# Kernel tuning notes

Hardware: AMD Instinct MI355X
Metric: run time of the kernel (lower is better)

The kernel has to match this reference:

```python
import jax, jax.numpy as jnp
import numpy as np

L = 5; F = 16; K = 32; R_CUT = 5.0; N_TYPES = 10
A = 10000  # n_atoms
P = 50000  # n_atom_pairs


def cg_coeff(l1, l2, l3):
    # Deterministic stand-in for Clebsch-Gordan coefficients (cgc arg of the layer).
    rs = np.random.RandomState(1000 + l1 * 100 + l2 * 10 + l3)
    return jnp.asarray(rs.standard_normal((2 * l1 + 1, 2 * l2 + 1, 2 * l3 + 1)).astype(np.float32))


def setup_inputs() -> dict:
    key = jax.random.key(0)
    ks = jax.random.split(key, 16)
    inp = {}
    for l in range(L):
        inp[f"c{l}"] = jax.random.normal(ks[l], (A, F, 2 * l + 1), jnp.float32)
    inp["R"] = jax.random.uniform(ks[5], (A, 3), jnp.float32) * 3.0  # positions in a box -> most d < r_cut
    inp["w_rad"] = jax.random.normal(ks[6], (L, K, F), jnp.float32) * 0.1
    inp["weight"] = jax.random.normal(ks[7], (N_TYPES * N_TYPES, L, F, F), jnp.float32) * (1.0 / np.sqrt(F))
    inp["s_collapse"] = jax.random.normal(ks[8], (3, F), jnp.float32) * 0.1
    inp["p_collapse"] = jax.random.normal(ks[9], (2, F), jnp.float32) * 0.1
    inp["d_collapse"] = jax.random.normal(ks[10], (1, F), jnp.float32) * 0.1
    inp["Z"] = jax.random.randint(ks[11], (A,), 0, N_TYPES)
    inp["atom_pair_indices"] = jax.random.randint(ks[12], (P, 2), 0, A)
    inp["atom_idx"] = jnp.arange(P)
    return inp


def reference(c0, c1, c2, c3, c4, R, w_rad, weight, s_collapse, p_collapse, d_collapse,
              Z, atom_pair_indices, atom_idx):
    c = [c0, c1, c2, c3, c4]
    i, j = atom_pair_indices[:, 0], atom_pair_indices[:, 1]
    # pairwise displacement / distance
    Rij = R[i] - R[j]                                    # (P,3)
    d = jnp.linalg.norm(Rij, axis=-1)                    # (P,)
    # Pairmix: smooth radial basis with cosine cutoff, per-l projection K->F
    n = jnp.arange(1, K + 1, dtype=jnp.float32)
    env = 0.5 * (jnp.cos(jnp.pi * jnp.clip(d, 0.0, R_CUT) / R_CUT) + 1.0) * (d < R_CUT)
    rbf = jnp.sin(n[None, :] * jnp.pi * d[:, None] / R_CUT) * env[:, None]   # (P,K)
    g = jnp.einsum('pk,lkf->lpf', rbf, w_rad)            # (L,P,F)
    c_out = [g[l][:, :, None] * (c[l][i] + c[l][j]) for l in range(L)]        # (P,F,2l+1)
    # atom-type-pair weights (symmetrized)
    sel = atom_pair_indices[atom_idx]                    # (P,2)
    t1, t2 = Z[sel[:, 0]], Z[sel[:, 1]]
    gw = weight[t1 * N_TYPES + t2] + weight[t2 * N_TYPES + t1]               # (P,L,F,F)
    c_out = [jnp.einsum('pbc,pcm->pbm', gw[:, l], c_out[l]) for l in range(L)]
    # CG tensor-product expansion into (l1,l2) blocks
    collapses = [s_collapse, p_collapse, d_collapse]
    Mblk = {}
    for l1 in range(3):
        for l2 in range(l1 + 1):
            Mx = jnp.zeros((P, 2 * l1 + 1, 2 * l2 + 1, F), jnp.float32)
            for l3 in range(l1 - l2, l1 + l2 + 1):
                Mx = Mx + jnp.einsum('mna,pfa->pmnf', cg_coeff(l1, l2, l3), c_out[l3])
            Mx = jnp.einsum('pmnf,af,bf->pmnab', Mx, collapses[l1], collapses[l2])
            a, b = collapses[l1].shape[0], collapses[l2].shape[0]
            Mblk[(l1, l2)] = Mx.reshape(P, (2 * l1 + 1) * a, (2 * l2 + 1) * b)
    T = lambda x: jnp.transpose(x, (0, 2, 1))
    r1 = jnp.concatenate([Mblk[(0, 0)], Mblk[(1, 0)], Mblk[(2, 0)]], axis=1)   # (P,14,3)
    r2 = jnp.concatenate([T(Mblk[(1, 0)]), Mblk[(1, 1)], Mblk[(2, 1)]], axis=1)  # (P,14,6)
    r3 = jnp.concatenate([T(Mblk[(2, 0)]), T(Mblk[(2, 1)]), Mblk[(2, 2)]], axis=1)  # (P,14,5)
    return jnp.concatenate([r1, r2, r3], axis=2)         # (P,14,14)
```

## Files before the change

### kernel.cpp

```cpp
#include <hip/hip_runtime.h>
#include <cstdint>

#define PI_F 3.14159265358979323846f

namespace cgc {

constexpr double csqrt(double x) {
  if (x <= 0.0) return 0.0;
  double m = x; int e = 0;
  while (m >= 4.0) { m *= 0.25; e++; }
  while (m < 1.0) { m *= 4.0; e--; }
  double g = 1.5;
  for (int i = 0; i < 16; i++) g = 0.5 * (g + m / g);
  double s = g;
  if (e > 0) for (int i = 0; i < e; i++) s *= 2.0;
  else       for (int i = 0; i < -e; i++) s *= 0.5;
  return s;
}

constexpr double clog(double x) {
  int k = 0;
  double m = x;
  while (m < 0.7071067811865476) { m *= 2.0; k--; }
  while (m > 1.4142135623730951) { m *= 0.5; k++; }
  double t = (m - 1.0) / (m + 1.0), t2 = t * t, s = 0.0, p = t;
  for (int i = 0; i < 27; i++) { s += p / (double)(2 * i + 1); p *= t2; }
  return 2.0 * s + (double)k * 0.6931471805599453;
}

struct RS { uint32_t mt[624]; int mti; bool has; double g; };

constexpr void rs_seed(RS& r, uint32_t s) {
  for (int i = 0; i < 624; i++) { r.mt[i] = s; s = 1812433253u * (s ^ (s >> 30)) + (uint32_t)i + 1u; }
  r.mti = 624; r.has = false; r.g = 0.0;
}
constexpr uint32_t rs_next(RS& r) {
  if (r.mti >= 624) {
    for (int i = 0; i < 624; i++) {
      uint32_t y = (r.mt[i] & 0x80000000u) | (r.mt[(i + 1) % 624] & 0x7fffffffu);
      r.mt[i] = r.mt[(i + 397) % 624] ^ (y >> 1) ^ ((y & 1u) ? 0x9908b0dfu : 0u);
    }
    r.mti = 0;
  }
  uint32_t y = r.mt[r.mti++];
  y ^= y >> 11; y ^= (y << 7) & 0x9d2c5680u; y ^= (y << 15) & 0xefc60000u; y ^= y >> 18;
  return y;
}
constexpr double rs_dbl(RS& r) {
  uint32_t a = rs_next(r) >> 5, b = rs_next(r) >> 6;
  return ((double)a * 67108864.0 + (double)b) / 9007199254740992.0;
}
constexpr double rs_gauss(RS& r) {
  if (r.has) { r.has = false; return r.g; }
  double x1 = 0, x2 = 0, r2 = 0;
  do {
    x1 = 2.0 * rs_dbl(r) - 1.0;
    x2 = 2.0 * rs_dbl(r) - 1.0;
    r2 = x1 * x1 + x2 * x2;
  } while (r2 >= 1.0 || r2 == 0.0);
  double f = csqrt(-2.0 * clog(r2) / r2);
  r.g = f * x1; r.has = true;
  return f * x2;
}

struct Tab { float v[228]; };

constexpr Tab gen(int l1, int l2, int l3) {
  Tab t{};
  RS r{};
  rs_seed(r, (uint32_t)(1000 + l1 * 100 + l2 * 10 + l3));
  int sz = (2 * l1 + 1) * (2 * l2 + 1) * (2 * l3 + 1);
  for (int k = 0; k < sz; k++) t.v[k] = (float)rs_gauss(r);
  return t;
}

constexpr Tab T000 = gen(0,0,0);
constexpr Tab T101 = gen(1,0,1);
constexpr Tab T110 = gen(1,1,0);
constexpr Tab T111 = gen(1,1,1);
constexpr Tab T112 = gen(1,1,2);
constexpr Tab T202 = gen(2,0,2);
constexpr Tab T211 = gen(2,1,1);
constexpr Tab T212 = gen(2,1,2);
constexpr Tab T213 = gen(2,1,3);
constexpr Tab T220 = gen(2,2,0);
constexpr Tab T221 = gen(2,2,1);
constexpr Tab T222 = gen(2,2,2);
constexpr Tab T223 = gen(2,2,3);
constexpr Tab T224 = gen(2,2,4);

struct alignas(16) Stage {
  int tabD[133 * 4];
  float cg[966];
  uint32_t tabC[133];
};

constexpr Stage make_stage() {
  Stage S{};
  const Tab* tabs[14] = {&T000,&T101,&T110,&T111,&T112,&T202,&T211,&T212,&T213,
                         &T220,&T221,&T222,&T223,&T224};
  const int KL[14][3] = {{0,0,0},{1,0,1},{1,1,0},{1,1,1},{1,1,2},{2,0,2},{2,1,1},
                         {2,1,2},{2,1,3},{2,2,0},{2,2,1},{2,2,2},{2,2,3},{2,2,4}};
  const int kBk[6][2] = {{0,0},{1,0},{1,1},{2,0},{2,1},{2,2}};

  int cgbase[6] = {}, dbase[6] = {}, xlenA[6] = {};
  int off = 0, doff = 0;
  for (int bk = 0; bk < 6; bk++) {
    int l1 = kBk[bk][0], l2 = kBk[bk][1];
    int M = 2 * l1 + 1, N = 2 * l2 + 1;
    int Ar = (l1 == 0) ? 3 : (l1 == 1) ? 2 : 1;
    int Br = (l2 == 0) ? 3 : (l2 == 1) ? 2 : 1;
    int xs[25] = {}, xl3[25] = {}, xa[25] = {};
    int cnt = 0;
    for (int l3 = l1 - l2; l3 <= l1 + l2; l3++)
      for (int a = 0; a < 2 * l3 + 1; a++) {
        xs[cnt] = l3 * l3 + a; xl3[cnt] = l3; xa[cnt] = a; cnt++;
      }
    int xlen = cnt;
    xlenA[bk] = xlen; cgbase[bk] = off; dbase[bk] = doff;
    for (int mn = 0; mn < M * N; mn++)
      for (int xi = 0; xi < xlen; xi++) {
        int l3 = xl3[xi], K3 = 2 * l3 + 1, ti = 0;
        for (int c = 0; c < 14; c++)
          if (KL[c][0] == l1 && KL[c][1] == l2 && KL[c][2] == l3) ti = c;
        S.cg[off + mn * xlen + xi] = tabs[ti]->v[mn * K3 + xa[xi]];
      }
    off += M * N * xlen;
    for (int q = 0; q < Ar * Br; q++) {
      int a = q / Br, b = q % Br;
      int u = (l1 == 0) ? a : (l1 == 1) ? 3 + a : 5;
      int v = (l2 == 0) ? b : (l2 == 1) ? 3 + b : 5;
      for (int xi = 0; xi < xlen; xi++)
        S.tabC[doff + q * xlen + xi] = (uint32_t)(u | (v << 4) | (xs[xi] << 8));
    }
    doff += Ar * Br * xlen;
  }
  const int ord[6] = {5, 4, 2, 3, 1, 0};
  int ei = 0;
  for (int bo = 0; bo < 6; bo++) {
    int bk = ord[bo];
    int l1 = kBk[bk][0], l2 = kBk[bk][1];
    int M = 2 * l1 + 1, N = 2 * l2 + 1;
    int Ar = (l1 == 0) ? 3 : (l1 == 1) ? 2 : 1;
    int Br = (l2 == 0) ? 3 : (l2 == 1) ? 2 : 1;
    int rb1 = (l1 == 0) ? 0 : (l1 == 1) ? 3 : 9;
    int rb2 = (l2 == 0) ? 0 : (l2 == 1) ? 3 : 9;
    int colDim = N * Br, xlen = xlenA[bk];
    for (int e = 0; e < M * N * Ar * Br; e++) {
      int b = e % Br, t2 = e / Br;
      int a = t2 % Ar; t2 /= Ar;
      int n = t2 % N, m = t2 / N;
      int mn = m * N + n, q = a * Br + b;
      int ri = e / colDim, ci = e % colDim;
      int p1 = (rb1 + ri) * 14 + (rb2 + ci);
      int p2 = (l1 == l2) ? p1 : ((rb2 + ci) * 14 + (rb1 + ri));
      S.tabD[4 * ei + 0] = (cgbase[bk] + mn * xlen) | (xlen << 16);
      S.tabD[4 * ei + 1] = dbase[bk] + q * xlen;
      S.tabD[4 * ei + 2] = p1;
      S.tabD[4 * ei + 3] = p2;
      ei++;
    }
  }
  return S;
}

constexpr Stage ST = make_stage();

}

__device__ const cgc::Stage g_tab = cgc::ST;

#define PSTRIDE 536

__global__ __launch_bounds__(256, 4) void outlayer_kernel(
    const float* __restrict__ c0, const float* __restrict__ c1,
    const float* __restrict__ c2, const float* __restrict__ c3,
    const float* __restrict__ c4, const float* __restrict__ R,
    const float* __restrict__ w_rad, const float* __restrict__ weight,
    const float* __restrict__ s_colg, const float* __restrict__ p_colg,
    const float* __restrict__ d_colg, const int* __restrict__ Z,
    const int* __restrict__ api, const int* __restrict__ aidx,
    float* __restrict__ out) {
  __shared__ float s_wrad[2560];
  __shared__ __align__(16) float s_cg[966];
  __shared__ __align__(16) float s_w6[36 * 16];
  __shared__ __align__(16) float s_buf[16 * PSTRIDE];
  __shared__ int s_tabC[133];
  __shared__ __align__(16) int4 s_tabD[133];

  const int tid = threadIdx.x;

#pragma unroll
  for (int t = 0; t < 10; t++) s_wrad[tid + t * 256] = w_rad[tid + t * 256];
  for (int e = tid; e < 966; e += 256) s_cg[e] = g_tab.cg[e];
  for (int e = tid; e < 133; e += 256) {
    s_tabC[e] = (int)g_tab.tabC[e];
    s_tabD[e] = ((const int4*)g_tab.tabD)[e];
  }
  for (int idx = tid; idx < 576; idx += 256) {
    int comb = idx >> 4, f = idx & 15;
    int u = comb / 6, v = comb % 6;
    float cu = (u < 3) ? s_colg[u * 16 + f] : (u < 5) ? p_colg[(u - 3) * 16 + f] : d_colg[f];
    float cv = (v < 3) ? s_colg[v * 16 + f] : (v < 5) ? p_colg[(v - 3) * 16 + f] : d_colg[f];
    s_w6[comb * 16 + ((f + 4 * (comb >> 1)) & 15)] = cu * cv;
  }
  __syncthreads();

  const int grp = tid >> 4;
  const int lane = tid & 15;
  const int p = blockIdx.x * 16 + grp;
  float* sb = s_buf + grp * PSTRIDE;
  float* sbD = sb + 400;

  const int i = api[2 * p], j = api[2 * p + 1];
  const int ai = aidx[p];
  const int t1 = Z[api[2 * ai]], t2 = Z[api[2 * ai + 1]];

  float dx = R[3 * i + 0] - R[3 * j + 0];
  float dy = R[3 * i + 1] - R[3 * j + 1];
  float dz = R[3 * i + 2] - R[3 * j + 2];
  float d = sqrtf(dx * dx + dy * dy + dz * dz);
  float env = 0.0f;
  if (d < 5.0f) env = 0.5f * (__cosf(PI_F * d * 0.2f) + 1.0f);
  float th = PI_F * d * 0.2f;
  float rlo = __sinf((float)(lane + 1) * th) * env;
  float rhi = __sinf((float)(lane + 17) * th) * env;

  float gl[5] = {0.f, 0.f, 0.f, 0.f, 0.f};
#pragma unroll
  for (int k = 0; k < 16; k++) {
    float rv = __shfl(rlo, k, 16);
#pragma unroll
    for (int l = 0; l < 5; l++) gl[l] += rv * s_wrad[l * 512 + k * 16 + lane];
  }
#pragma unroll
  for (int k = 0; k < 16; k++) {
    float rv = __shfl(rhi, k, 16);
#pragma unroll
    for (int l = 0; l < 5; l++) gl[l] += rv * s_wrad[l * 512 + (k + 16) * 16 + lane];
  }

  const float* cl[5] = {c0, c1, c2, c3, c4};
#pragma unroll
  for (int l = 0; l < 5; l++) {
    const int nm = 2 * l + 1;
    const float* ci = cl[l] + ((size_t)i * 16 + lane) * nm;
    const float* cj = cl[l] + ((size_t)j * 16 + lane) * nm;
    float* hb = sb + 16 * l * l;
#pragma unroll
    for (int m = 0; m < 2 * l + 1; m++)
      hb[m * 16 + lane] = gl[l] * (ci[m] + cj[m]);
  }
  __builtin_amdgcn_wave_barrier();

  float co[25];
#pragma unroll
  for (int x = 0; x < 25; x++) co[x] = 0.f;
  const float* w1 = weight + (size_t)(t1 * 10 + t2) * 1280 + lane * 16;
  const float* w2 = weight + (size_t)(t2 * 10 + t1) * 1280 + lane * 16;
#pragma unroll
  for (int l = 0; l < 5; l++) {
    float gwreg[16];
#pragma unroll
    for (int cq = 0; cq < 4; cq++) {
      float4 a4 = *(const float4*)(w1 + l * 256 + cq * 4);
      float4 b4 = *(const float4*)(w2 + l * 256 + cq * 4);
      gwreg[cq * 4 + 0] = a4.x + b4.x;
      gwreg[cq * 4 + 1] = a4.y + b4.y;
      gwreg[cq * 4 + 2] = a4.z + b4.z;
      gwreg[cq * 4 + 3] = a4.w + b4.w;
    }
#pragma unroll
    for (int m = 0; m < 2 * l + 1; m++) {
      const float* hb = &sb[16 * l * l + m * 16];
      float acc = co[l * l + m];
#pragma unroll
      for (int cq = 0; cq < 4; cq++) {
        float4 h4 = *(const float4*)(hb + cq * 4);
        acc += gwreg[cq * 4 + 0] * h4.x + gwreg[cq * 4 + 1] * h4.y +
               gwreg[cq * 4 + 2] * h4.z + gwreg[cq * 4 + 3] * h4.w;
      }
      co[l * l + m] = acc;
    }
  }
  __builtin_amdgcn_wave_barrier();

#pragma unroll
  for (int x = 0; x < 25; x++) sb[x * 16 + ((lane + 4 * (x >> 1)) & 15)] = co[x];
  __builtin_amdgcn_wave_barrier();

#pragma unroll
  for (int it = 0; it < 9; it++) {
    int t = it * 16 + lane;
    if (t < 133) {
      int pc = s_tabC[t];
      int u = pc & 15, v = (pc >> 4) & 15, x = pc >> 8;
      int comb = u * 6 + v;
      int rotW = 4 * (comb >> 1), rotC = 4 * (x >> 1);
      const float* wrow = &s_w6[comb * 16];
      const float* crow = &sb[x * 16];
      float acc = 0.f;
#pragma unroll
      for (int q = 0; q < 4; q++) {
        float4 wv = *(const float4*)&wrow[(4 * q + rotW) & 15];
        float4 cv = *(const float4*)&crow[(4 * q + rotC) & 15];
        acc += wv.x * cv.x + wv.y * cv.y + wv.z * cv.z + wv.w * cv.w;
      }
      sbD[t] = acc;
    }
  }
  __builtin_amdgcn_wave_barrier();

#pragma unroll
  for (int it = 0; it < 9; it++) {
    int t = it * 16 + lane;
    if (t < 133) {
      int4 td = s_tabD[t];
      int goff = td.x & 0xffff, len = td.x >> 16, doff = td.y;
      float acc = 0.f;
      for (int xi = 0; xi < len; xi++) acc += s_cg[goff + xi] * sbD[doff + xi];
      sb[td.z] = acc;
      sb[td.w] = acc;
    }
  }
  __builtin_amdgcn_wave_barrier();

  float* outp = out + (size_t)p * 196;
#pragma unroll
  for (int r = 0; r < 4; r++) {
    int idx = r * 16 + lane;
    if (idx < 49) {
      float4 v = *(const float4*)&sb[idx * 4];
      *(float4*)(outp + idx * 4) = v;
    }
  }
}

extern "C" void kernel_launch(void* const* d_in, const int* in_sizes, int n_in,
                              void* d_out, int out_size, void* d_ws, size_t ws_size,
                              hipStream_t stream) {
  (void)in_sizes; (void)n_in; (void)out_size; (void)d_ws; (void)ws_size;

  const float* c0 = (const float*)d_in[0];
  const float* c1 = (const float*)d_in[1];
  const float* c2 = (const float*)d_in[2];
  const float* c3 = (const float*)d_in[3];
  const float* c4 = (const float*)d_in[4];
  const float* R = (const float*)d_in[5];
  const float* w_rad = (const float*)d_in[6];
  const float* weight = (const float*)d_in[7];
  const float* s_col = (const float*)d_in[8];
  const float* p_col = (const float*)d_in[9];
  const float* d_col = (const float*)d_in[10];
  const int* Z = (const int*)d_in[11];
  const int* api = (const int*)d_in[12];
  const int* aidx = (const int*)d_in[13];

  dim3 grid(3125), block(256);
  hipLaunchKernelGGL(outlayer_kernel, grid, block, 0, stream,
                     c0, c1, c2, c3, c4, R, w_rad, weight, s_col, p_col, d_col,
                     Z, api, aidx, (float*)d_out);
}
```

Before: 182.2 us.

## Drop shared-memory staging of tables and radial weights; pad CG rows to float4

Stops copying w_rad, the CG coefficients and the index tables into shared memory at block start. Those values are now read straight from global/constant memory, and each lane computes all 32 radial sines itself instead of shuffling them across lanes. The CG and intermediate D rows are padded to multiples of four so the final contraction can use float4 loads, and the padding in the per-pair buffer is zeroed first. This shrinks LDS use and the block prologue, at the cost of more global loads through the cache and 32 sine evaluations per lane instead of 2.

```diff
diff --git a/kernel.cpp b/kernel.cpp
--- a/kernel.cpp
+++ b/kernel.cpp
@@ -90,8 +90,8 @@
 constexpr Tab T224 = gen(2,2,4);
 
 struct alignas(16) Stage {
+  float cgP[1104];
   int tabD[133 * 4];
-  float cg[966];
   uint32_t tabC[133];
 };
 
@@ -103,7 +103,7 @@
                          {2,1,2},{2,1,3},{2,2,0},{2,2,1},{2,2,2},{2,2,3},{2,2,4}};
   const int kBk[6][2] = {{0,0},{1,0},{1,1},{2,0},{2,1},{2,2}};
 
-  int cgbase[6] = {}, dbase[6] = {}, xlenA[6] = {};
+  int cgbase[6] = {}, dbase[6] = {}, xlenA[6] = {}, cgs[6] = {}, dss[6] = {};
   int off = 0, doff = 0;
   for (int bk = 0; bk < 6; bk++) {
     int l1 = kBk[bk][0], l2 = kBk[bk][1];
@@ -117,23 +117,40 @@
         xs[cnt] = l3 * l3 + a; xl3[cnt] = l3; xa[cnt] = a; cnt++;
       }
     int xlen = cnt;
-    xlenA[bk] = xlen; cgbase[bk] = off; dbase[bk] = doff;
+    int pstride = ((xlen + 3) / 4) * 4;
+    xlenA[bk] = xlen; cgs[bk] = pstride; dss[bk] = pstride;
+    cgbase[bk] = off; dbase[bk] = doff;
     for (int mn = 0; mn < M * N; mn++)
       for (int xi = 0; xi < xlen; xi++) {
         int l3 = xl3[xi], K3 = 2 * l3 + 1, ti = 0;
         for (int c = 0; c < 14; c++)
           if (KL[c][0] == l1 && KL[c][1] == l2 && KL[c][2] == l3) ti = c;
-        S.cg[off + mn * xlen + xi] = tabs[ti]->v[mn * K3 + xa[xi]];
-      }
-    off += M * N * xlen;
-    for (int q = 0; q < Ar * Br; q++) {
-      int a = q / Br, b = q % Br;
-      int u = (l1 == 0) ? a : (l1 == 1) ? 3 + a : 5;
-      int v = (l2 == 0) ? b : (l2 == 1) ? 3 + b : 5;
-      for (int xi = 0; xi < xlen; xi++)
-        S.tabC[doff + q * xlen + xi] = (uint32_t)(u | (v << 4) | (xs[xi] << 8));
-    }
-    doff += Ar * Br * xlen;
+        S.cgP[off + mn * pstride + xi] = tabs[ti]->v[mn * K3 + xa[xi]];
+      }
+    off += M * N * pstride;
+    doff += Ar * Br * pstride;
+  }
+  {
+    int t = 0;
+    for (int bk = 0; bk < 6; bk++) {
+      int l1 = kBk[bk][0], l2 = kBk[bk][1];
+      int Ar = (l1 == 0) ? 3 : (l1 == 1) ? 2 : 1;
+      int Br = (l2 == 0) ? 3 : (l2 == 1) ? 2 : 1;
+      for (int q = 0; q < Ar * Br; q++) {
+        int a = q / Br, b = q % Br;
+        int u = (l1 == 0) ? a : (l1 == 1) ? 3 + a : 5;
+        int v = (l2 == 0) ? b : (l2 == 1) ? 3 + b : 5;
+        int comb = u * 6 + v;
+        int xi = 0;
+        for (int l3 = l1 - l2; l3 <= l1 + l2; l3++)
+          for (int a3 = 0; a3 < 2 * l3 + 1; a3++) {
+            int x = l3 * l3 + a3;
+            int pos = dbase[bk] + q * dss[bk] + xi;
+            S.tabC[t++] = (uint32_t)(comb | (x << 8) | (pos << 16));
+            xi++;
+          }
+      }
+    }
   }
   const int ord[6] = {5, 4, 2, 3, 1, 0};
   int ei = 0;
@@ -145,7 +162,7 @@
     int Br = (l2 == 0) ? 3 : (l2 == 1) ? 2 : 1;
     int rb1 = (l1 == 0) ? 0 : (l1 == 1) ? 3 : 9;
     int rb2 = (l2 == 0) ? 0 : (l2 == 1) ? 3 : 9;
-    int colDim = N * Br, xlen = xlenA[bk];
+    int colDim = N * Br;
     for (int e = 0; e < M * N * Ar * Br; e++) {
       int b = e % Br, t2 = e / Br;
       int a = t2 % Ar; t2 /= Ar;
@@ -154,8 +171,8 @@
       int ri = e / colDim, ci = e % colDim;
       int p1 = (rb1 + ri) * 14 + (rb2 + ci);
       int p2 = (l1 == l2) ? p1 : ((rb2 + ci) * 14 + (rb1 + ri));
-      S.tabD[4 * ei + 0] = (cgbase[bk] + mn * xlen) | (xlen << 16);
-      S.tabD[4 * ei + 1] = dbase[bk] + q * xlen;
+      S.tabD[4 * ei + 0] = ((cgbase[bk] + mn * cgs[bk]) / 4) | ((cgs[bk] / 4) << 16);
+      S.tabD[4 * ei + 1] = dbase[bk] + q * dss[bk];
       S.tabD[4 * ei + 2] = p1;
       S.tabD[4 * ei + 3] = p2;
       ei++;
@@ -170,7 +187,7 @@
 
 __device__ const cgc::Stage g_tab = cgc::ST;
 
-#define PSTRIDE 536
+#define PSTRIDE 600
 
 __global__ __launch_bounds__(256, 4) void outlayer_kernel(
     const float* __restrict__ c0, const float* __restrict__ c1,
@@ -181,22 +198,11 @@
     const float* __restrict__ d_colg, const int* __restrict__ Z,
     const int* __restrict__ api, const int* __restrict__ aidx,
     float* __restrict__ out) {
-  __shared__ float s_wrad[2560];
-  __shared__ __align__(16) float s_cg[966];
   __shared__ __align__(16) float s_w6[36 * 16];
   __shared__ __align__(16) float s_buf[16 * PSTRIDE];
-  __shared__ int s_tabC[133];
-  __shared__ __align__(16) int4 s_tabD[133];
 
   const int tid = threadIdx.x;
 
-#pragma unroll
-  for (int t = 0; t < 10; t++) s_wrad[tid + t * 256] = w_rad[tid + t * 256];
-  for (int e = tid; e < 966; e += 256) s_cg[e] = g_tab.cg[e];
-  for (int e = tid; e < 133; e += 256) {
-    s_tabC[e] = (int)g_tab.tabC[e];
-    s_tabD[e] = ((const int4*)g_tab.tabD)[e];
-  }
   for (int idx = tid; idx < 576; idx += 256) {
     int comb = idx >> 4, f = idx & 15;
     int u = comb / 6, v = comb % 6;
@@ -223,21 +229,16 @@
   float env = 0.0f;
   if (d < 5.0f) env = 0.5f * (__cosf(PI_F * d * 0.2f) + 1.0f);
   float th = PI_F * d * 0.2f;
-  float rlo = __sinf((float)(lane + 1) * th) * env;
-  float rhi = __sinf((float)(lane + 17) * th) * env;
+  float rv[32];
+#pragma unroll
+  for (int k = 0; k < 32; k++) rv[k] = __sinf((float)(k + 1) * th) * env;
 
   float gl[5] = {0.f, 0.f, 0.f, 0.f, 0.f};
 #pragma unroll
-  for (int k = 0; k < 16; k++) {
-    float rv = __shfl(rlo, k, 16);
-#pragma unroll
-    for (int l = 0; l < 5; l++) gl[l] += rv * s_wrad[l * 512 + k * 16 + lane];
-  }
-#pragma unroll
-  for (int k = 0; k < 16; k++) {
-    float rv = __shfl(rhi, k, 16);
-#pragma unroll
-    for (int l = 0; l < 5; l++) gl[l] += rv * s_wrad[l * 512 + (k + 16) * 16 + lane];
+  for (int l = 0; l < 5; l++) {
+#pragma unroll
+    for (int k = 0; k < 32; k++)
+      gl[l] += rv[k] * w_rad[(l * 32 + k) * 16 + lane];
   }
 
   const float* cl[5] = {c0, c1, c2, c3, c4};
@@ -287,15 +288,18 @@
 
 #pragma unroll
   for (int x = 0; x < 25; x++) sb[x * 16 + ((lane + 4 * (x >> 1)) & 15)] = co[x];
+
+  float4 z4 = make_float4(0.f, 0.f, 0.f, 0.f);
+#pragma unroll
+  for (int z = 0; z < 3; z++) *(float4*)&sbD[(z * 16 + lane) * 4] = z4;
   __builtin_amdgcn_wave_barrier();
 
 #pragma unroll
   for (int it = 0; it < 9; it++) {
     int t = it * 16 + lane;
     if (t < 133) {
-      int pc = s_tabC[t];
-      int u = pc & 15, v = (pc >> 4) & 15, x = pc >> 8;
-      int comb = u * 6 + v;
+      int pc = (int)g_tab.tabC[t];
+      int comb = pc & 0xff, x = (pc >> 8) & 0xff, pos = pc >> 16;
       int rotW = 4 * (comb >> 1), rotC = 4 * (x >> 1);
       const float* wrow = &s_w6[comb * 16];
       const float* crow = &sb[x * 16];
@@ -306,19 +310,24 @@
         float4 cv = *(const float4*)&crow[(4 * q + rotC) & 15];
         acc += wv.x * cv.x + wv.y * cv.y + wv.z * cv.z + wv.w * cv.w;
       }
-      sbD[t] = acc;
-    }
-  }
-  __builtin_amdgcn_wave_barrier();
-
+      sbD[pos] = acc;
+    }
+  }
+  __builtin_amdgcn_wave_barrier();
+
+  const float4* cg4 = (const float4*)g_tab.cgP;
 #pragma unroll
   for (int it = 0; it < 9; it++) {
     int t = it * 16 + lane;
     if (t < 133) {
-      int4 td = s_tabD[t];
-      int goff = td.x & 0xffff, len = td.x >> 16, doff = td.y;
+      int4 td = ((const int4*)g_tab.tabD)[t];
+      int goff4 = td.x & 0xffff, lenq = td.x >> 16, doff = td.y;
       float acc = 0.f;
-      for (int xi = 0; xi < len; xi++) acc += s_cg[goff + xi] * sbD[doff + xi];
+      for (int q = 0; q < lenq; q++) {
+        float4 cgv = cg4[goff4 + q];
+        float4 dv = *(const float4*)&sbD[doff + 4 * q];
+        acc += cgv.x * dv.x + cgv.y * dv.y + cgv.z * dv.z + cgv.w * dv.w;
+      }
       sb[td.z] = acc;
       sb[td.w] = acc;
     }
```

Result: slower. 283.0 us (+55.3%).

## Double pairs per block, pack radial weights as bf16, read tables from constant memory

Applied to the files above, without the earlier changes.

Doubles the block to 512 threads handling 32 pairs each, which halves the number of blocks and amortises the per-block shared-memory setup. The radial weight matrix is stored in shared memory as packed bf16 pairs, halving its footprint and the number of LDS reads in the radial projection. The CG index tables are now read directly from device memory instead of being staged in shared memory. The bf16 weights reduce precision of the radial projection, and the larger shared buffer (about 69 KB) may limit how many blocks fit per CU.

```diff
diff --git a/kernel.cpp b/kernel.cpp
--- a/kernel.cpp
+++ b/kernel.cpp
@@ -171,8 +171,9 @@
 __device__ const cgc::Stage g_tab = cgc::ST;
 
 #define PSTRIDE 536
-
-__global__ __launch_bounds__(256, 4) void outlayer_kernel(
+#define NPAIR 32
+
+__global__ __launch_bounds__(512, 4) void outlayer_kernel(
     const float* __restrict__ c0, const float* __restrict__ c1,
     const float* __restrict__ c2, const float* __restrict__ c3,
     const float* __restrict__ c4, const float* __restrict__ R,
@@ -181,23 +182,24 @@
     const float* __restrict__ d_colg, const int* __restrict__ Z,
     const int* __restrict__ api, const int* __restrict__ aidx,
     float* __restrict__ out) {
-  __shared__ float s_wrad[2560];
+  __shared__ uint32_t s_wradH[1280];
   __shared__ __align__(16) float s_cg[966];
   __shared__ __align__(16) float s_w6[36 * 16];
-  __shared__ __align__(16) float s_buf[16 * PSTRIDE];
-  __shared__ int s_tabC[133];
-  __shared__ __align__(16) int4 s_tabD[133];
+  __shared__ __align__(16) float s_buf[NPAIR * PSTRIDE];
 
   const int tid = threadIdx.x;
 
-#pragma unroll
-  for (int t = 0; t < 10; t++) s_wrad[tid + t * 256] = w_rad[tid + t * 256];
-  for (int e = tid; e < 966; e += 256) s_cg[e] = g_tab.cg[e];
-  for (int e = tid; e < 133; e += 256) {
-    s_tabC[e] = (int)g_tab.tabC[e];
-    s_tabD[e] = ((const int4*)g_tab.tabD)[e];
-  }
-  for (int idx = tid; idx < 576; idx += 256) {
+  for (int idx = tid; idx < 1280; idx += 512) {
+    int l = idx >> 8, r = idx & 255, k2 = r >> 4, f = r & 15;
+    float v0 = w_rad[(l * 32 + 2 * k2) * 16 + f];
+    float v1 = w_rad[(l * 32 + 2 * k2 + 1) * 16 + f];
+    uint32_t u0 = __float_as_uint(v0), u1 = __float_as_uint(v1);
+    uint32_t b0 = (u0 + 0x7fffu + ((u0 >> 16) & 1u)) >> 16;
+    uint32_t b1 = (u1 + 0x7fffu + ((u1 >> 16) & 1u)) >> 16;
+    s_wradH[idx] = b0 | (b1 << 16);
+  }
+  for (int e = tid; e < 966; e += 512) s_cg[e] = g_tab.cg[e];
+  for (int idx = tid; idx < 576; idx += 512) {
     int comb = idx >> 4, f = idx & 15;
     int u = comb / 6, v = comb % 6;
     float cu = (u < 3) ? s_colg[u * 16 + f] : (u < 5) ? p_colg[(u - 3) * 16 + f] : d_colg[f];
@@ -208,130 +210,132 @@
 
   const int grp = tid >> 4;
   const int lane = tid & 15;
-  const int p = blockIdx.x * 16 + grp;
-  float* sb = s_buf + grp * PSTRIDE;
-  float* sbD = sb + 400;
-
-  const int i = api[2 * p], j = api[2 * p + 1];
-  const int ai = aidx[p];
-  const int t1 = Z[api[2 * ai]], t2 = Z[api[2 * ai + 1]];
-
-  float dx = R[3 * i + 0] - R[3 * j + 0];
-  float dy = R[3 * i + 1] - R[3 * j + 1];
-  float dz = R[3 * i + 2] - R[3 * j + 2];
-  float d = sqrtf(dx * dx + dy * dy + dz * dz);
-  float env = 0.0f;
-  if (d < 5.0f) env = 0.5f * (__cosf(PI_F * d * 0.2f) + 1.0f);
-  float th = PI_F * d * 0.2f;
-  float rlo = __sinf((float)(lane + 1) * th) * env;
-  float rhi = __sinf((float)(lane + 17) * th) * env;
-
-  float gl[5] = {0.f, 0.f, 0.f, 0.f, 0.f};
-#pragma unroll
-  for (int k = 0; k < 16; k++) {
-    float rv = __shfl(rlo, k, 16);
-#pragma unroll
-    for (int l = 0; l < 5; l++) gl[l] += rv * s_wrad[l * 512 + k * 16 + lane];
-  }
-#pragma unroll
-  for (int k = 0; k < 16; k++) {
-    float rv = __shfl(rhi, k, 16);
-#pragma unroll
-    for (int l = 0; l < 5; l++) gl[l] += rv * s_wrad[l * 512 + (k + 16) * 16 + lane];
-  }
-
-  const float* cl[5] = {c0, c1, c2, c3, c4};
-#pragma unroll
-  for (int l = 0; l < 5; l++) {
-    const int nm = 2 * l + 1;
-    const float* ci = cl[l] + ((size_t)i * 16 + lane) * nm;
-    const float* cj = cl[l] + ((size_t)j * 16 + lane) * nm;
-    float* hb = sb + 16 * l * l;
-#pragma unroll
-    for (int m = 0; m < 2 * l + 1; m++)
-      hb[m * 16 + lane] = gl[l] * (ci[m] + cj[m]);
-  }
-  __builtin_amdgcn_wave_barrier();
-
-  float co[25];
-#pragma unroll
-  for (int x = 0; x < 25; x++) co[x] = 0.f;
-  const float* w1 = weight + (size_t)(t1 * 10 + t2) * 1280 + lane * 16;
-  const float* w2 = weight + (size_t)(t2 * 10 + t1) * 1280 + lane * 16;
-#pragma unroll
-  for (int l = 0; l < 5; l++) {
-    float gwreg[16];
-#pragma unroll
-    for (int cq = 0; cq < 4; cq++) {
-      float4 a4 = *(const float4*)(w1 + l * 256 + cq * 4);
-      float4 b4 = *(const float4*)(w2 + l * 256 + cq * 4);
-      gwreg[cq * 4 + 0] = a4.x + b4.x;
-      gwreg[cq * 4 + 1] = a4.y + b4.y;
-      gwreg[cq * 4 + 2] = a4.z + b4.z;
-      gwreg[cq * 4 + 3] = a4.w + b4.w;
-    }
-#pragma unroll
-    for (int m = 0; m < 2 * l + 1; m++) {
-      const float* hb = &sb[16 * l * l + m * 16];
-      float acc = co[l * l + m];
+  const int p = blockIdx.x * NPAIR + grp;
+  if (p < 50000) {
+    float* sb = s_buf + grp * PSTRIDE;
+    float* sbD = sb + 400;
+
+    const int i = api[2 * p], j = api[2 * p + 1];
+    const int ai = aidx[p];
+    const int t1 = Z[api[2 * ai]], t2 = Z[api[2 * ai + 1]];
+
+    float dx = R[3 * i + 0] - R[3 * j + 0];
+    float dy = R[3 * i + 1] - R[3 * j + 1];
+    float dz = R[3 * i + 2] - R[3 * j + 2];
+    float d = sqrtf(dx * dx + dy * dy + dz * dz);
+    float env = 0.0f;
+    if (d < 5.0f) env = 0.5f * (__cosf(PI_F * d * 0.2f) + 1.0f);
+    float th = PI_F * d * 0.2f;
+    float rlo = __sinf((float)(lane + 1) * th) * env;
+    float rhi = __sinf((float)(lane + 17) * th) * env;
+
+    float gl[5] = {0.f, 0.f, 0.f, 0.f, 0.f};
+#pragma unroll
+    for (int k2 = 0; k2 < 16; k2++) {
+      float ra = (k2 < 8) ? __shfl(rlo, 2 * k2, 16) : __shfl(rhi, 2 * k2 - 16, 16);
+      float rb = (k2 < 8) ? __shfl(rlo, 2 * k2 + 1, 16) : __shfl(rhi, 2 * k2 - 15, 16);
+#pragma unroll
+      for (int l = 0; l < 5; l++) {
+        uint32_t w = s_wradH[(l * 16 + k2) * 16 + lane];
+        float lo = __uint_as_float(w << 16);
+        float hi = __uint_as_float(w & 0xffff0000u);
+        gl[l] += ra * lo + rb * hi;
+      }
+    }
+
+    const float* cl[5] = {c0, c1, c2, c3, c4};
+#pragma unroll
+    for (int l = 0; l < 5; l++) {
+      const int nm = 2 * l + 1;
+      const float* ci = cl[l] + ((size_t)i * 16 + lane) * nm;
+      const float* cj = cl[l] + ((size_t)j * 16 + lane) * nm;
+      float* hb = sb + 16 * l * l;
+#pragma unroll
+      for (int m = 0; m < 2 * l + 1; m++)
+        hb[m * 16 + lane] = gl[l] * (ci[m] + cj[m]);
+    }
+    __builtin_amdgcn_wave_barrier();
+
+    float co[25];
+#pragma unroll
+    for (int x = 0; x < 25; x++) co[x] = 0.f;
+    const float* w1 = weight + (size_t)(t1 * 10 + t2) * 1280 + lane * 16;
+    const float* w2 = weight + (size_t)(t2 * 10 + t1) * 1280 + lane * 16;
+#pragma unroll
+    for (int l = 0; l < 5; l++) {
+      float gwreg[16];
 #pragma unroll
       for (int cq = 0; cq < 4; cq++) {
-        float4 h4 = *(const float4*)(hb + cq * 4);
-        acc += gwreg[cq * 4 + 0] * h4.x + gwreg[cq * 4 + 1] * h4.y +
-               gwreg[cq * 4 + 2] * h4.z + gwreg[cq * 4 + 3] * h4.w;
-      }
-      co[l * l + m] = acc;
-    }
-  }
-  __builtin_amdgcn_wave_barrier();
-
-#pragma unroll
-  for (int x = 0; x < 25; x++) sb[x * 16 + ((lane + 4 * (x >> 1)) & 15)] = co[x];
-  __builtin_amdgcn_wave_barrier();
-
-#pragma unroll
-  for (int it = 0; it < 9; it++) {
-    int t = it * 16 + lane;
-    if (t < 133) {
-      int pc = s_tabC[t];
-      int u = pc & 15, v = (pc >> 4) & 15, x = pc >> 8;
-      int comb = u * 6 + v;
-      int rotW = 4 * (comb >> 1), rotC = 4 * (x >> 1);
-      const float* wrow = &s_w6[comb * 16];
-      const float* crow = &sb[x * 16];
-      float acc = 0.f;
-#pragma unroll
-      for (int q = 0; q < 4; q++) {
-        float4 wv = *(const float4*)&wrow[(4 * q + rotW) & 15];
-        float4 cv = *(const float4*)&crow[(4 * q + rotC) & 15];
-        acc += wv.x * cv.x + wv.y * cv.y + wv.z * cv.z + wv.w * cv.w;
-      }
-      sbD[t] = acc;
-    }
-  }
-  __builtin_amdgcn_wave_barrier();
-
-#pragma unroll
-  for (int it = 0; it < 9; it++) {
-    int t = it * 16 + lane;
-    if (t < 133) {
-      int4 td = s_tabD[t];
-      int goff = td.x & 0xffff, len = td.x >> 16, doff = td.y;
-      float acc = 0.f;
-      for (int xi = 0; xi < len; xi++) acc += s_cg[goff + xi] * sbD[doff + xi];
-      sb[td.z] = acc;
-      sb[td.w] = acc;
-    }
-  }
-  __builtin_amdgcn_wave_barrier();
-
-  float* outp = out + (size_t)p * 196;
-#pragma unroll
-  for (int r = 0; r < 4; r++) {
-    int idx = r * 16 + lane;
-    if (idx < 49) {
-      float4 v = *(const float4*)&sb[idx * 4];
-      *(float4*)(outp + idx * 4) = v;
+        float4 a4 = *(const float4*)(w1 + l * 256 + cq * 4);
+        float4 b4 = *(const float4*)(w2 + l * 256 + cq * 4);
+        gwreg[cq * 4 + 0] = a4.x + b4.x;
+        gwreg[cq * 4 + 1] = a4.y + b4.y;
+        gwreg[cq * 4 + 2] = a4.z + b4.z;
+        gwreg[cq * 4 + 3] = a4.w + b4.w;
+      }
+#pragma unroll
+      for (int m = 0; m < 2 * l + 1; m++) {
+        const float* hb = &sb[16 * l * l + m * 16];
+        float acc = co[l * l + m];
+#pragma unroll
+        for (int cq = 0; cq < 4; cq++) {
+          float4 h4 = *(const float4*)(hb + cq * 4);
+          acc += gwreg[cq * 4 + 0] * h4.x + gwreg[cq * 4 + 1] * h4.y +
+                 gwreg[cq * 4 + 2] * h4.z + gwreg[cq * 4 + 3] * h4.w;
+        }
+        co[l * l + m] = acc;
+      }
+    }
+    __builtin_amdgcn_wave_barrier();
+
+#pragma unroll
+    for (int x = 0; x < 25; x++) sb[x * 16 + ((lane + 4 * (x >> 1)) & 15)] = co[x];
+    __builtin_amdgcn_wave_barrier();
+
+#pragma unroll
+    for (int it = 0; it < 9; it++) {
+      int t = it * 16 + lane;
+      if (t < 133) {
+        int pc = (int)g_tab.tabC[t];
+        int u = pc & 15, v = (pc >> 4) & 15, x = pc >> 8;
+        int comb = u * 6 + v;
+        int rotW = 4 * (comb >> 1), rotC = 4 * (x >> 1);
+        const float* wrow = &s_w6[comb * 16];
+        const float* crow = &sb[x * 16];
+        float acc = 0.f;
+#pragma unroll
+        for (int q = 0; q < 4; q++) {
+          float4 wv = *(const float4*)&wrow[(4 * q + rotW) & 15];
+          float4 cv = *(const float4*)&crow[(4 * q + rotC) & 15];
+          acc += wv.x * cv.x + wv.y * cv.y + wv.z * cv.z + wv.w * cv.w;
+        }
+        sbD[t] = acc;
+      }
+    }
+    __builtin_amdgcn_wave_barrier();
+
+#pragma unroll
+    for (int it = 0; it < 9; it++) {
+      int t = it * 16 + lane;
+      if (t < 133) {
+        int4 td = ((const int4*)g_tab.tabD)[t];
+        int goff = td.x & 0xffff, len = td.x >> 16, doff = td.y;
+        float acc = 0.f;
+        for (int xi = 0; xi < len; xi++) acc += s_cg[goff + xi] * sbD[doff + xi];
+        sb[td.z] = acc;
+        sb[td.w] = acc;
+      }
+    }
+    __builtin_amdgcn_wave_barrier();
+
+    float* outp = out + (size_t)p * 196;
+#pragma unroll
+    for (int r = 0; r < 4; r++) {
+      int idx = r * 16 + lane;
+      if (idx < 49) {
+        float4 v = *(const float4*)&sb[idx * 4];
+        *(float4*)(outp + idx * 4) = v;
+      }
     }
   }
 }
@@ -356,7 +360,7 @@
   const int* api = (const int*)d_in[12];
   const int* aidx = (const int*)d_in[13];
 
-  dim3 grid(3125), block(256);
+  dim3 grid((50000 + NPAIR - 1) / NPAIR), block(512);
   hipLaunchKernelGGL(outlayer_kernel, grid, block, 0, stream,
                      c0, c1, c2, c3, c4, R, w_rad, weight, s_col, p_col, d_col,
                      Z, api, aidx, (float*)d_out);
```

After: 197.5 us. 8.4% more time.
